# Kernel tuning notes

Measured on AMD Instinct MI355X. Metric: run time of the kernel, lower is better.

Reference implementation:

```python
import jax, jax.numpy as jnp
import numpy as np

EMBED = 256
HEADS = 8
LEVELS = 4
POINTS = 8
HD = EMBED // HEADS  # 32


def setup_inputs() -> dict:
    key = jax.random.key(0)
    ks = jax.random.split(key, 12)
    bs, nq = 1, 22500
    shapes = np.array([[100, 100], [50, 50], [25, 25], [13, 13]], dtype=np.int32)
    areas = shapes[:, 0] * shapes[:, 1]
    nv = int(areas.sum())  # 13294
    lsi = np.concatenate([[0], np.cumsum(areas)[:-1]]).astype(np.int32)
    s = 1.0 / np.sqrt(EMBED)
    return {
        "query": jax.random.normal(ks[0], (bs, nq, EMBED), jnp.float32),
        "value": jax.random.normal(ks[1], (bs, nv, EMBED), jnp.float32),
        "reference_points": jax.random.uniform(ks[2], (bs, nq, LEVELS, 2), jnp.float32),
        "spatial_shapes": shapes,          # static int metadata
        "level_start_index": lsi,          # static int metadata
        "W_value": jax.random.normal(ks[3], (EMBED, EMBED), jnp.float32) * s,
        "b_value": jax.random.normal(ks[4], (EMBED,), jnp.float32) * 0.01,
        "W_off": jax.random.normal(ks[5], (EMBED, HEADS * LEVELS * POINTS * 2), jnp.float32) * s,
        "b_off": jax.random.normal(ks[6], (HEADS * LEVELS * POINTS * 2,), jnp.float32) * 0.5,
        "W_attn": jax.random.normal(ks[7], (EMBED, HEADS * LEVELS * POINTS), jnp.float32) * s,
        "b_attn": jax.random.normal(ks[8], (HEADS * LEVELS * POINTS,), jnp.float32) * 0.01,
        "W_out": jax.random.normal(ks[9], (EMBED, EMBED), jnp.float32) * s,
        "b_out": jax.random.normal(ks[10], (EMBED,), jnp.float32) * 0.01,
    }


def _bilinear(img, xy):
    # img: (B, H, W, C); xy: (B, N, 2) normalized to [0,1], align_corners=False,
    # zero padding for out-of-range samples (matches F.grid_sample in the torch fallback).
    B, H, W, C = img.shape
    x = xy[..., 0] * W - 0.5
    y = xy[..., 1] * H - 0.5
    x0f = jnp.floor(x)
    y0f = jnp.floor(y)
    wx = (x - x0f)[..., None]
    wy = (y - y0f)[..., None]
    x0 = x0f.astype(jnp.int32)
    y0 = y0f.astype(jnp.int32)
    flat = img.reshape(B, H * W, C)

    def g(yi, xi):
        valid = ((yi >= 0) & (yi < H) & (xi >= 0) & (xi < W)).astype(img.dtype)
        idx = jnp.clip(yi, 0, H - 1) * W + jnp.clip(xi, 0, W - 1)
        return jnp.take_along_axis(flat, idx[..., None], axis=1) * valid[..., None]

    v00 = g(y0, x0)
    v01 = g(y0, x0 + 1)
    v10 = g(y0 + 1, x0)
    v11 = g(y0 + 1, x0 + 1)
    return (v00 * (1 - wy) * (1 - wx) + v01 * (1 - wy) * wx
            + v10 * wy * (1 - wx) + v11 * wy * wx)


def reference(query, value, reference_points, spatial_shapes, level_start_index,
              W_value, b_value, W_off, b_off, W_attn, b_attn, W_out, b_out):
    bs, nq, _ = query.shape
    # value projection -> per-head values (bs, nv, H, hd)
    v = (value @ W_value + b_value).reshape(bs, -1, HEADS, HD)
    # sampling offsets (bs, nq, H, L, P, 2) and attention weights softmaxed over L*P
    off = (query @ W_off + b_off).reshape(bs, nq, HEADS, LEVELS, POINTS, 2)
    aw = jax.nn.softmax((query @ W_attn + b_attn).reshape(bs, nq, HEADS, LEVELS * POINTS), -1)
    aw = aw.reshape(bs, nq, HEADS, LEVELS, POINTS)
    ss = np.asarray(spatial_shapes)
    norm = jnp.asarray(np.stack([ss[:, 1], ss[:, 0]], -1).astype(np.float32))  # (L, 2) as (W, H)
    loc = reference_points[:, :, None, :, None, :] + off / norm[None, None, None, :, None, :]
    out = jnp.zeros((bs, nq, HEADS, HD), query.dtype)
    start = 0
    for l in range(LEVELS):
        H, W = int(ss[l, 0]), int(ss[l, 1])
        vl = v[:, start:start + H * W].reshape(bs, H, W, HEADS, HD)
        vl = vl.transpose(0, 3, 1, 2, 4).reshape(bs * HEADS, H, W, HD)
        ll = loc[:, :, :, l].transpose(0, 2, 1, 3, 4).reshape(bs * HEADS, nq * POINTS, 2)
        samp = _bilinear(vl, ll).reshape(bs, HEADS, nq, POINTS, HD)
        out = out + jnp.einsum('bhqp,bhqpd->bqhd', aw[:, :, :, l].transpose(0, 2, 1, 3), samp)
        start += H * W
    out = out.reshape(bs, nq, EMBED) @ W_out + b_out
    return query + out  # identity residual (identity defaults to query)
```

## Files before the change

### kernel.cpp

```cpp
#include <hip/hip_runtime.h>
#include <hip/hip_bf16.h>
#include <cstdint>

#define NQ 22500
#define NV 13294
#define EMBED 256

typedef short bf16x8 __attribute__((ext_vector_type(8)));
typedef float f32x4  __attribute__((ext_vector_type(4)));

__device__ __forceinline__ int lvlH(int l) { return l==0?100 : l==1?50 : l==2?25 : 13; }
__device__ __forceinline__ int lvlW(int l) { return l==0?100 : l==1?50 : l==2?25 : 13; }
__device__ __forceinline__ int lvlStart(int l) { return l==0?0 : l==1?10000 : l==2?12500 : 13125; }

__device__ __forceinline__ ushort f2bf(float x) {
    uint32_t u = __float_as_uint(x);
    uint32_t r = (u + 0x7FFFu + ((u >> 16) & 1u)) >> 16;
    return (ushort)r;
}

__global__ __launch_bounds__(256) void prep_kernel(
    const float* __restrict__ value, const float* __restrict__ query,
    const float* __restrict__ Wv, const float* __restrict__ Wo,
    const float* __restrict__ Wa, const float* __restrict__ Wt,
    ushort* __restrict__ val_bf, ushort* __restrict__ q_bf,
    ushort* __restrict__ Wv_t, ushort* __restrict__ Wo_t,
    ushort* __restrict__ Wa_t, ushort* __restrict__ Wt_t)
{
    const int y = blockIdx.y;
    const int idx0 = blockIdx.x * 256 + threadIdx.x;
    const int stride = gridDim.x * 256;

    if (y == 0) {
        for (int i = idx0; i < (NV * 256) / 4; i += stride) {
            float4 v = ((const float4*)value)[i];
            ushort4 o; o.x = f2bf(v.x); o.y = f2bf(v.y); o.z = f2bf(v.z); o.w = f2bf(v.w);
            ((ushort4*)val_bf)[i] = o;
        }
    } else if (y == 1) {
        for (int i = idx0; i < (NQ * 256) / 4; i += stride) {
            float4 v = ((const float4*)query)[i];
            ushort4 o; o.x = f2bf(v.x); o.y = f2bf(v.y); o.z = f2bf(v.z); o.w = f2bf(v.w);
            ((ushort4*)q_bf)[i] = o;
        }
    } else if (y == 2) {
        for (int i = idx0; i < 256 * 256; i += stride) {
            int n = i & 255, k = i >> 8;
            Wv_t[n * 256 + k] = f2bf(Wv[k * 256 + n]);
        }
    } else if (y == 3) {
        for (int i = idx0; i < 512 * 256; i += stride) {
            int n = i & 511, k = i >> 9;
            Wo_t[n * 256 + k] = f2bf(Wo[k * 512 + n]);
        }
    } else if (y == 4) {
        for (int i = idx0; i < 256 * 256; i += stride) {
            int n = i & 255, k = i >> 8;
            Wa_t[n * 256 + k] = f2bf(Wa[k * 256 + n]);
        }
    } else {
        for (int i = idx0; i < 256 * 256; i += stride) {
            int n = i & 255, k = i >> 8;
            Wt_t[n * 256 + k] = f2bf(Wt[k * 256 + n]);
        }
    }
}

template<bool RESID, bool OUT_BF16>
__global__ __launch_bounds__(256) void gemm_bf16(
    const ushort* __restrict__ A,
    const ushort* __restrict__ Bt,
    const float* __restrict__ bias, const float* __restrict__ R,
    void* __restrict__ Cv, int M, int N)
{
    __shared__ __align__(16) ushort As[128][72];
    __shared__ __align__(16) ushort Bs[64][72];

    const int tid  = threadIdx.x;
    const int row0 = blockIdx.x * 128;
    const int col0 = blockIdx.y * 64;
    const int wave = tid >> 6, lane = tid & 63;
    const int r = lane & 15, g = lane >> 4;

    const int ar = tid >> 1, ac = (tid & 1) * 32;
    const int br = tid >> 2, bc = (tid & 3) * 16;
    const bool aok = (row0 + ar) < M;
    const ushort* Aptr = A + (size_t)(row0 + ar) * 256 + ac;
    const ushort* Bptr = Bt + (size_t)(col0 + br) * 256 + bc;

    f32x4 acc[2][4] = {};

    for (int k0 = 0; k0 < 256; k0 += 64) {
        uint4 av[4], bv[2];
#pragma unroll
        for (int j = 0; j < 4; ++j)
            av[j] = aok ? *(const uint4*)(Aptr + k0 + j * 8) : make_uint4(0, 0, 0, 0);
#pragma unroll
        for (int j = 0; j < 2; ++j)
            bv[j] = *(const uint4*)(Bptr + k0 + j * 8);

#pragma unroll
        for (int j = 0; j < 4; ++j)
            *(uint4*)&As[ar][ac + j * 8] = av[j];
#pragma unroll
        for (int j = 0; j < 2; ++j)
            *(uint4*)&Bs[br][bc + j * 8] = bv[j];
        __syncthreads();

#pragma unroll
        for (int kk = 0; kk < 2; ++kk) {
            const int kc = kk * 32 + g * 8;
            bf16x8 a0 = *(const bf16x8*)&As[wave * 32 + r][kc];
            bf16x8 a1 = *(const bf16x8*)&As[wave * 32 + 16 + r][kc];
            bf16x8 b0 = *(const bf16x8*)&Bs[r][kc];
            bf16x8 b1 = *(const bf16x8*)&Bs[16 + r][kc];
            bf16x8 b2 = *(const bf16x8*)&Bs[32 + r][kc];
            bf16x8 b3 = *(const bf16x8*)&Bs[48 + r][kc];

            acc[0][0] = __builtin_amdgcn_mfma_f32_16x16x32_bf16(a0, b0, acc[0][0], 0, 0, 0);
            acc[0][1] = __builtin_amdgcn_mfma_f32_16x16x32_bf16(a0, b1, acc[0][1], 0, 0, 0);
            acc[0][2] = __builtin_amdgcn_mfma_f32_16x16x32_bf16(a0, b2, acc[0][2], 0, 0, 0);
            acc[0][3] = __builtin_amdgcn_mfma_f32_16x16x32_bf16(a0, b3, acc[0][3], 0, 0, 0);
            acc[1][0] = __builtin_amdgcn_mfma_f32_16x16x32_bf16(a1, b0, acc[1][0], 0, 0, 0);
            acc[1][1] = __builtin_amdgcn_mfma_f32_16x16x32_bf16(a1, b1, acc[1][1], 0, 0, 0);
            acc[1][2] = __builtin_amdgcn_mfma_f32_16x16x32_bf16(a1, b2, acc[1][2], 0, 0, 0);
            acc[1][3] = __builtin_amdgcn_mfma_f32_16x16x32_bf16(a1, b3, acc[1][3], 0, 0, 0);
        }
        __syncthreads();
    }

#pragma unroll
    for (int mi = 0; mi < 2; ++mi)
#pragma unroll
        for (int ni = 0; ni < 4; ++ni) {
            const int col = col0 + ni * 16 + r;
            const float bb = bias[col];
#pragma unroll
            for (int j = 0; j < 4; ++j) {
                const int row = row0 + wave * 32 + mi * 16 + g * 4 + j;
                if (row < M) {
                    float o = acc[mi][ni][j] + bb;
                    if (RESID) o += R[(size_t)row * N + col];
                    if (OUT_BF16)
                        ((ushort*)Cv)[(size_t)row * N + col] = f2bf(o);
                    else
                        ((float*)Cv)[(size_t)row * N + col] = o;
                }
            }
        }
}

__device__ __forceinline__ void fma8(float* acc, uint4 u, float w) {
    acc[0] += w * __uint_as_float(u.x << 16);
    acc[1] += w * __uint_as_float(u.x & 0xffff0000u);
    acc[2] += w * __uint_as_float(u.y << 16);
    acc[3] += w * __uint_as_float(u.y & 0xffff0000u);
    acc[4] += w * __uint_as_float(u.z << 16);
    acc[5] += w * __uint_as_float(u.z & 0xffff0000u);
    acc[6] += w * __uint_as_float(u.w << 16);
    acc[7] += w * __uint_as_float(u.w & 0xffff0000u);
}

__global__ __launch_bounds__(256) void sample_kernel(
    const ushort* __restrict__ v,
    const float* __restrict__ off_raw,
    const float* __restrict__ attn_raw,
    const float* __restrict__ rp,
    ushort* __restrict__ agg)
{
    __shared__ int4   idxs[8][32];
    __shared__ float4 wts[8][32];

    const int q    = blockIdx.x;
    const int tid  = threadIdx.x;
    const int h    = tid >> 5;
    const int lane = tid & 31;
    const int l    = lane >> 3;
    const int p    = lane & 7;

    const float ox = off_raw[(size_t)q * 512 + h * 64 + l * 16 + p * 2 + 0];
    const float oy = off_raw[(size_t)q * 512 + h * 64 + l * 16 + p * 2 + 1];
    const float rx = rp[(size_t)q * 8 + l * 2 + 0];
    const float ry = rp[(size_t)q * 8 + l * 2 + 1];
    const float Wl = (float)lvlW(l), Hl = (float)lvlH(l);
    const int   Wi = lvlW(l), Hi = lvlH(l), base = lvlStart(l);
    const float xf = rx * Wl + ox - 0.5f;
    const float yf = ry * Hl + oy - 0.5f;

    float logit = attn_raw[(size_t)q * 256 + h * 32 + lane];
    float m = logit;
#pragma unroll
    for (int s = 16; s; s >>= 1) m = fmaxf(m, __shfl_xor(m, s, 32));
    float e = __expf(logit - m);
    float ssum = e;
#pragma unroll
    for (int s = 16; s; s >>= 1) ssum += __shfl_xor(ssum, s, 32);
    const float w = e / ssum;

    const float x0f = floorf(xf), y0f = floorf(yf);
    const float fx = xf - x0f, fy = yf - y0f;
    const int x0 = (int)x0f, y0 = (int)y0f;
    const int x1 = x0 + 1, y1 = y0 + 1;

    const bool vx0 = (unsigned)x0 < (unsigned)Wi;
    const bool vx1 = (unsigned)x1 < (unsigned)Wi;
    const bool vy0 = (unsigned)y0 < (unsigned)Hi;
    const bool vy1 = (unsigned)y1 < (unsigned)Hi;
    const int cx0 = vx0 ? x0 : 0, cx1 = vx1 ? x1 : 0;
    const int cy0 = vy0 ? y0 : 0, cy1 = vy1 ? y1 : 0;

    int4 idx;
    idx.x = base + cy0 * Wi + cx0;
    idx.y = base + cy0 * Wi + cx1;
    idx.z = base + cy1 * Wi + cx0;
    idx.w = base + cy1 * Wi + cx1;
    float4 wv;
    wv.x = (vy0 && vx0) ? w * (1.f - fy) * (1.f - fx) : 0.f;
    wv.y = (vy0 && vx1) ? w * (1.f - fy) * fx         : 0.f;
    wv.z = (vy1 && vx0) ? w * fy * (1.f - fx)         : 0.f;
    wv.w = (vy1 && vx1) ? w * fy * fx                 : 0.f;

    idxs[h][lane] = idx;
    wts[h][lane]  = wv;
    __syncthreads();

    const int slot = lane & 7;
    const int cg   = lane >> 3;
    const ushort* vbase = v + h * 32 + cg * 8;

    float acc[8] = {};
#pragma unroll
    for (int i = 0; i < 4; ++i) {
        const int s = slot + i * 8;
        const int4   id = idxs[h][s];
        const float4 ww = wts[h][s];
        uint4 c00 = *(const uint4*)(vbase + (size_t)id.x * 256);
        uint4 c01 = *(const uint4*)(vbase + (size_t)id.y * 256);
        uint4 c10 = *(const uint4*)(vbase + (size_t)id.z * 256);
        uint4 c11 = *(const uint4*)(vbase + (size_t)id.w * 256);
        fma8(acc, c00, ww.x);
        fma8(acc, c01, ww.y);
        fma8(acc, c10, ww.z);
        fma8(acc, c11, ww.w);
    }

#pragma unroll
    for (int m8 = 1; m8 <= 4; m8 <<= 1)
#pragma unroll
        for (int j = 0; j < 8; ++j)
            acc[j] += __shfl_xor(acc[j], m8, 32);

    if (slot == 0) {
        ushort pk[8];
#pragma unroll
        for (int j = 0; j < 8; ++j) pk[j] = f2bf(acc[j]);
        *(uint4*)(agg + (size_t)q * 256 + h * 32 + cg * 8) = *(const uint4*)pk;
    }
}

extern "C" void kernel_launch(void* const* d_in, const int* in_sizes, int n_in,
                              void* d_out, int out_size, void* d_ws, size_t ws_size,
                              hipStream_t stream)
{
    const float* query   = (const float*)d_in[0];
    const float* value   = (const float*)d_in[1];
    const float* rp      = (const float*)d_in[2];
    const float* W_value = (const float*)d_in[5];
    const float* b_value = (const float*)d_in[6];
    const float* W_off   = (const float*)d_in[7];
    const float* b_off   = (const float*)d_in[8];
    const float* W_attn  = (const float*)d_in[9];
    const float* b_attn  = (const float*)d_in[10];
    const float* W_out   = (const float*)d_in[11];
    const float* b_out   = (const float*)d_in[12];
    float* out = (float*)d_out;

    ushort* v_bf    = (ushort*)d_ws;
    float*  off_ws  = (float*)(v_bf + (size_t)NV * 256);
    float*  attn_ws = off_ws + (size_t)NQ * 512;
    ushort* q_bf    = (ushort*)(attn_ws + (size_t)NQ * 256);
    ushort* val_bf  = q_bf + (size_t)NQ * 256;
    ushort* Wv_t    = val_bf + (size_t)NV * 256;
    ushort* Wo_t    = Wv_t + 256 * 256;
    ushort* Wa_t    = Wo_t + 512 * 256;
    ushort* Wt_t    = Wa_t + 256 * 256;
    ushort* agg_bf  = q_bf;

    dim3 blk(256);

    prep_kernel<<<dim3(2048, 6), blk, 0, stream>>>(
        value, query, W_value, W_off, W_attn, W_out,
        val_bf, q_bf, Wv_t, Wo_t, Wa_t, Wt_t);

    gemm_bf16<false, true><<<dim3((NV + 127) / 128, 4), blk, 0, stream>>>(
        val_bf, Wv_t, b_value, nullptr, v_bf, NV, 256);
    gemm_bf16<false, false><<<dim3((NQ + 127) / 128, 8), blk, 0, stream>>>(
        q_bf, Wo_t, b_off, nullptr, off_ws, NQ, 512);
    gemm_bf16<false, false><<<dim3((NQ + 127) / 128, 4), blk, 0, stream>>>(
        q_bf, Wa_t, b_attn, nullptr, attn_ws, NQ, 256);
    sample_kernel<<<NQ, blk, 0, stream>>>(v_bf, off_ws, attn_ws, rp, agg_bf);
    gemm_bf16<true, false><<<dim3((NQ + 127) / 128, 4), blk, 0, stream>>>(
        agg_bf, Wt_t, b_out, query, out, NQ, 256);
}
```

Before: 342.9 us.

## Fuse fp32-to-bf16 conversion into GEMMs, merge offset/attn GEMMs, fp32 value sampling

Removes the separate activation conversion pass by having the GEMM load fp32 A tiles and pack them to bf16 in registers. It concatenates the offset and attention-logit weights into one 768-column GEMM so query is read once. The value projection is now stored in fp32, and the sampler gathers float4 per lane and reduces across slots with fewer shuffles. The trade-off is twice the bytes per value gather and a larger fp32 value workspace, in exchange for fewer kernel launches and less conversion traffic.

Result: faster. 308.2 us (-10.1%).

```diff
diff --git a/kernel.cpp b/kernel.cpp
--- a/kernel.cpp
+++ b/kernel.cpp
@@ -18,57 +18,46 @@
     uint32_t r = (u + 0x7FFFu + ((u >> 16) & 1u)) >> 16;
     return (ushort)r;
 }
-
-__global__ __launch_bounds__(256) void prep_kernel(
-    const float* __restrict__ value, const float* __restrict__ query,
+__device__ __forceinline__ uint32_t pk2(float lo, float hi) {
+    return (uint32_t)f2bf(lo) | ((uint32_t)f2bf(hi) << 16);
+}
+
+__global__ __launch_bounds__(256) void prep_w(
     const float* __restrict__ Wv, const float* __restrict__ Wo,
     const float* __restrict__ Wa, const float* __restrict__ Wt,
-    ushort* __restrict__ val_bf, ushort* __restrict__ q_bf,
-    ushort* __restrict__ Wv_t, ushort* __restrict__ Wo_t,
-    ushort* __restrict__ Wa_t, ushort* __restrict__ Wt_t)
+    const float* __restrict__ b_off, const float* __restrict__ b_attn,
+    ushort* __restrict__ Wv_t, ushort* __restrict__ Woa_t,
+    ushort* __restrict__ Wt_t, float* __restrict__ bias_oa)
 {
     const int y = blockIdx.y;
     const int idx0 = blockIdx.x * 256 + threadIdx.x;
     const int stride = gridDim.x * 256;
 
     if (y == 0) {
-        for (int i = idx0; i < (NV * 256) / 4; i += stride) {
-            float4 v = ((const float4*)value)[i];
-            ushort4 o; o.x = f2bf(v.x); o.y = f2bf(v.y); o.z = f2bf(v.z); o.w = f2bf(v.w);
-            ((ushort4*)val_bf)[i] = o;
+        for (int i = idx0; i < 256 * 256; i += stride) {
+            int n = i >> 8, k = i & 255;
+            Wv_t[n * 256 + k] = f2bf(Wv[k * 256 + n]);
         }
     } else if (y == 1) {
-        for (int i = idx0; i < (NQ * 256) / 4; i += stride) {
-            float4 v = ((const float4*)query)[i];
-            ushort4 o; o.x = f2bf(v.x); o.y = f2bf(v.y); o.z = f2bf(v.z); o.w = f2bf(v.w);
-            ((ushort4*)q_bf)[i] = o;
+        for (int i = idx0; i < 768 * 256; i += stride) {
+            int n = i >> 8, k = i & 255;
+            float w = (n < 512) ? Wo[k * 512 + n] : Wa[k * 256 + (n - 512)];
+            Woa_t[n * 256 + k] = f2bf(w);
         }
     } else if (y == 2) {
         for (int i = idx0; i < 256 * 256; i += stride) {
-            int n = i & 255, k = i >> 8;
-            Wv_t[n * 256 + k] = f2bf(Wv[k * 256 + n]);
-        }
-    } else if (y == 3) {
-        for (int i = idx0; i < 512 * 256; i += stride) {
-            int n = i & 511, k = i >> 9;
-            Wo_t[n * 256 + k] = f2bf(Wo[k * 512 + n]);
-        }
-    } else if (y == 4) {
-        for (int i = idx0; i < 256 * 256; i += stride) {
-            int n = i & 255, k = i >> 8;
-            Wa_t[n * 256 + k] = f2bf(Wa[k * 256 + n]);
+            int n = i >> 8, k = i & 255;
+            Wt_t[n * 256 + k] = f2bf(Wt[k * 256 + n]);
         }
     } else {
-        for (int i = idx0; i < 256 * 256; i += stride) {
-            int n = i & 255, k = i >> 8;
-            Wt_t[n * 256 + k] = f2bf(Wt[k * 256 + n]);
-        }
-    }
-}
-
-template<bool RESID, bool OUT_BF16>
+        for (int i = idx0; i < 768; i += stride)
+            bias_oa[i] = (i < 512) ? b_off[i] : b_attn[i - 512];
+    }
+}
+
+template<bool A_F32, bool RESID, bool OUT_BF16>
 __global__ __launch_bounds__(256) void gemm_bf16(
-    const ushort* __restrict__ A,
+    const void* __restrict__ Av,
     const ushort* __restrict__ Bt,
     const float* __restrict__ bias, const float* __restrict__ R,
     void* __restrict__ Cv, int M, int N)
@@ -85,16 +74,32 @@
     const int ar = tid >> 1, ac = (tid & 1) * 32;
     const int br = tid >> 2, bc = (tid & 3) * 16;
     const bool aok = (row0 + ar) < M;
-    const ushort* Aptr = A + (size_t)(row0 + ar) * 256 + ac;
+
+    const float*  Af = (const float*)Av;
+    const ushort* Ab = (const ushort*)Av;
+    const size_t  abase = (size_t)(row0 + ar) * 256 + ac;
     const ushort* Bptr = Bt + (size_t)(col0 + br) * 256 + bc;
 
     f32x4 acc[2][4] = {};
 
     for (int k0 = 0; k0 < 256; k0 += 64) {
         uint4 av[4], bv[2];
-#pragma unroll
-        for (int j = 0; j < 4; ++j)
-            av[j] = aok ? *(const uint4*)(Aptr + k0 + j * 8) : make_uint4(0, 0, 0, 0);
+        if (A_F32) {
+#pragma unroll
+            for (int j = 0; j < 4; ++j) {
+                if (aok) {
+                    float4 f0 = *(const float4*)(Af + abase + k0 + j * 8);
+                    float4 f1 = *(const float4*)(Af + abase + k0 + j * 8 + 4);
+                    av[j].x = pk2(f0.x, f0.y); av[j].y = pk2(f0.z, f0.w);
+                    av[j].z = pk2(f1.x, f1.y); av[j].w = pk2(f1.z, f1.w);
+                } else av[j] = make_uint4(0, 0, 0, 0);
+            }
+        } else {
+#pragma unroll
+            for (int j = 0; j < 4; ++j)
+                av[j] = aok ? *(const uint4*)(Ab + abase + k0 + j * 8)
+                            : make_uint4(0, 0, 0, 0);
+        }
 #pragma unroll
         for (int j = 0; j < 2; ++j)
             bv[j] = *(const uint4*)(Bptr + k0 + j * 8);
@@ -150,21 +155,9 @@
         }
 }
 
-__device__ __forceinline__ void fma8(float* acc, uint4 u, float w) {
-    acc[0] += w * __uint_as_float(u.x << 16);
-    acc[1] += w * __uint_as_float(u.x & 0xffff0000u);
-    acc[2] += w * __uint_as_float(u.y << 16);
-    acc[3] += w * __uint_as_float(u.y & 0xffff0000u);
-    acc[4] += w * __uint_as_float(u.z << 16);
-    acc[5] += w * __uint_as_float(u.z & 0xffff0000u);
-    acc[6] += w * __uint_as_float(u.w << 16);
-    acc[7] += w * __uint_as_float(u.w & 0xffff0000u);
-}
-
 __global__ __launch_bounds__(256) void sample_kernel(
-    const ushort* __restrict__ v,
-    const float* __restrict__ off_raw,
-    const float* __restrict__ attn_raw,
+    const float* __restrict__ v,
+    const float* __restrict__ oa,
     const float* __restrict__ rp,
     ushort* __restrict__ agg)
 {
@@ -178,8 +171,8 @@
     const int l    = lane >> 3;
     const int p    = lane & 7;
 
-    const float ox = off_raw[(size_t)q * 512 + h * 64 + l * 16 + p * 2 + 0];
-    const float oy = off_raw[(size_t)q * 512 + h * 64 + l * 16 + p * 2 + 1];
+    const float ox = oa[(size_t)q * 768 + h * 64 + l * 16 + p * 2 + 0];
+    const float oy = oa[(size_t)q * 768 + h * 64 + l * 16 + p * 2 + 1];
     const float rx = rp[(size_t)q * 8 + l * 2 + 0];
     const float ry = rp[(size_t)q * 8 + l * 2 + 1];
     const float Wl = (float)lvlW(l), Hl = (float)lvlH(l);
@@ -187,7 +180,7 @@
     const float xf = rx * Wl + ox - 0.5f;
     const float yf = ry * Hl + oy - 0.5f;
 
-    float logit = attn_raw[(size_t)q * 256 + h * 32 + lane];
+    float logit = oa[(size_t)q * 768 + 512 + h * 32 + lane];
     float m = logit;
 #pragma unroll
     for (int s = 16; s; s >>= 1) m = fmaxf(m, __shfl_xor(m, s, 32));
@@ -224,37 +217,38 @@
     wts[h][lane]  = wv;
     __syncthreads();
 
-    const int slot = lane & 7;
-    const int cg   = lane >> 3;
-    const ushort* vbase = v + h * 32 + cg * 8;
-
-    float acc[8] = {};
-#pragma unroll
-    for (int i = 0; i < 4; ++i) {
-        const int s = slot + i * 8;
+    const int slot = lane >> 3;
+    const int cg   = lane & 7;
+    const float* vbase = v + h * 32 + cg * 4;
+
+    float4 acc = make_float4(0.f, 0.f, 0.f, 0.f);
+#pragma unroll
+    for (int i = 0; i < 8; ++i) {
+        const int s = slot + i * 4;
         const int4   id = idxs[h][s];
         const float4 ww = wts[h][s];
-        uint4 c00 = *(const uint4*)(vbase + (size_t)id.x * 256);
-        uint4 c01 = *(const uint4*)(vbase + (size_t)id.y * 256);
-        uint4 c10 = *(const uint4*)(vbase + (size_t)id.z * 256);
-        uint4 c11 = *(const uint4*)(vbase + (size_t)id.w * 256);
-        fma8(acc, c00, ww.x);
-        fma8(acc, c01, ww.y);
-        fma8(acc, c10, ww.z);
-        fma8(acc, c11, ww.w);
-    }
-
-#pragma unroll
-    for (int m8 = 1; m8 <= 4; m8 <<= 1)
-#pragma unroll
-        for (int j = 0; j < 8; ++j)
-            acc[j] += __shfl_xor(acc[j], m8, 32);
+        const float4 v00 = *(const float4*)(vbase + (size_t)id.x * 256);
+        const float4 v01 = *(const float4*)(vbase + (size_t)id.y * 256);
+        const float4 v10 = *(const float4*)(vbase + (size_t)id.z * 256);
+        const float4 v11 = *(const float4*)(vbase + (size_t)id.w * 256);
+        acc.x += ww.x * v00.x + ww.y * v01.x + ww.z * v10.x + ww.w * v11.x;
+        acc.y += ww.x * v00.y + ww.y * v01.y + ww.z * v10.y + ww.w * v11.y;
+        acc.z += ww.x * v00.z + ww.y * v01.z + ww.z * v10.z + ww.w * v11.z;
+        acc.w += ww.x * v00.w + ww.y * v01.w + ww.z * v10.w + ww.w * v11.w;
+    }
+
+#pragma unroll
+    for (int s = 8; s <= 16; s <<= 1) {
+        acc.x += __shfl_xor(acc.x, s, 32);
+        acc.y += __shfl_xor(acc.y, s, 32);
+        acc.z += __shfl_xor(acc.z, s, 32);
+        acc.w += __shfl_xor(acc.w, s, 32);
+    }
 
     if (slot == 0) {
-        ushort pk[8];
-#pragma unroll
-        for (int j = 0; j < 8; ++j) pk[j] = f2bf(acc[j]);
-        *(uint4*)(agg + (size_t)q * 256 + h * 32 + cg * 8) = *(const uint4*)pk;
+        ushort4 pk;
+        pk.x = f2bf(acc.x); pk.y = f2bf(acc.y); pk.z = f2bf(acc.z); pk.w = f2bf(acc.w);
+        *(ushort4*)(agg + (size_t)q * 256 + h * 32 + cg * 4) = pk;
     }
 }
 
@@ -275,30 +269,25 @@
     const float* b_out   = (const float*)d_in[12];
     float* out = (float*)d_out;
 
-    ushort* v_bf    = (ushort*)d_ws;
-    float*  off_ws  = (float*)(v_bf + (size_t)NV * 256);
-    float*  attn_ws = off_ws + (size_t)NQ * 512;
-    ushort* q_bf    = (ushort*)(attn_ws + (size_t)NQ * 256);
-    ushort* val_bf  = q_bf + (size_t)NQ * 256;
-    ushort* Wv_t    = val_bf + (size_t)NV * 256;
-    ushort* Wo_t    = Wv_t + 256 * 256;
-    ushort* Wa_t    = Wo_t + 512 * 256;
-    ushort* Wt_t    = Wa_t + 256 * 256;
-    ushort* agg_bf  = q_bf;
+    float*  v_ws    = (float*)d_ws;
+    float*  oa_ws   = v_ws + (size_t)NV * 256;
+    ushort* agg_bf  = (ushort*)(oa_ws + (size_t)NQ * 768);
+    ushort* Wv_t    = agg_bf + (size_t)NQ * 256;
+    ushort* Woa_t   = Wv_t + 256 * 256;
+    ushort* Wt_t    = Woa_t + 768 * 256;
+    float*  bias_oa = (float*)(Wt_t + 256 * 256);
 
     dim3 blk(256);
 
-    prep_kernel<<<dim3(2048, 6), blk, 0, stream>>>(
-        value, query, W_value, W_off, W_attn, W_out,
-        val_bf, q_bf, Wv_t, Wo_t, Wa_t, Wt_t);
-
-    gemm_bf16<false, true><<<dim3((NV + 127) / 128, 4), blk, 0, stream>>>(
-        val_bf, Wv_t, b_value, nullptr, v_bf, NV, 256);
-    gemm_bf16<false, false><<<dim3((NQ + 127) / 128, 8), blk, 0, stream>>>(
-        q_bf, Wo_t, b_off, nullptr, off_ws, NQ, 512);
-    gemm_bf16<false, false><<<dim3((NQ + 127) / 128, 4), blk, 0, stream>>>(
-        q_bf, Wa_t, b_attn, nullptr, attn_ws, NQ, 256);
-    sample_kernel<<<NQ, blk, 0, stream>>>(v_bf, off_ws, attn_ws, rp, agg_bf);
-    gemm_bf16<true, false><<<dim3((NQ + 127) / 128, 4), blk, 0, stream>>>(
+    prep_w<<<dim3(128, 4), blk, 0, stream>>>(
+        W_value, W_off, W_attn, W_out, b_off, b_attn,
+        Wv_t, Woa_t, Wt_t, bias_oa);
+
+    gemm_bf16<true, false, false><<<dim3((NV + 127) / 128, 4), blk, 0, stream>>>(
+        value, Wv_t, b_value, nullptr, v_ws, NV, 256);
+    gemm_bf16<true, false, false><<<dim3((NQ + 127) / 128, 12), blk, 0, stream>>>(
+        query, Woa_t, bias_oa, nullptr, oa_ws, NQ, 768);
+    sample_kernel<<<NQ, blk, 0, stream>>>(v_ws, oa_ws, rp, agg_bf);
+    gemm_bf16<false, true, false><<<dim3((NQ + 127) / 128, 4), blk, 0, stream>>>(
         agg_bf, Wt_t, b_out, query, out, NQ, 256);
 }
```
